# Kernel tuning notes

Hardware: AMD Instinct MI355X
Metric: run time of the kernel (lower is better)

## Reference

```python
import jax, jax.numpy as jnp
import numpy as np

D_MODEL = 1024
NUM_HEADS = 16
D_K = D_MODEL // NUM_HEADS
SCALE = 1.0 / np.sqrt(D_K).astype(np.float32)
MASK_FILL = -10000.0


def setup_inputs() -> dict:
    key = jax.random.key(0)
    ks = jax.random.split(key, 5)
    B, S = 2, 2048
    x = jax.random.normal(ks[0], (B, S, D_MODEL), dtype=jnp.float32)
    mask = jax.random.randint(ks[1], (B, S), 0, 2, dtype=jnp.int32)
    # Kaiming-uniform-ish init like nn.Linear defaults
    lim1 = 1.0 / np.sqrt(D_MODEL)
    Wqkv = jax.random.uniform(ks[2], (D_MODEL, 3 * D_MODEL), jnp.float32, -lim1, lim1)
    bqkv = jnp.zeros((3 * D_MODEL,), jnp.float32)
    Wout = jax.random.uniform(ks[3], (D_MODEL, D_MODEL), jnp.float32, -lim1, lim1)
    bout = jnp.zeros((D_MODEL,), jnp.float32)
    return {"x": x, "mask": mask, "Wqkv": Wqkv, "bqkv": bqkv, "Wout": Wout, "bout": bout}


def reference(x, mask, Wqkv, bqkv, Wout, bout):
    B, S, _ = x.shape
    qkv = (x @ Wqkv + bqkv).reshape(B, S, 3, NUM_HEADS, D_K)
    qkv = jnp.transpose(qkv, (2, 0, 3, 1, 4))
    q, k, v = qkv[0], qkv[1], qkv[2]
    # scaled dot-product scores [B,H,S,S]
    scores = jnp.einsum("bhqd,bhkd->bhqk", q, k) * SCALE
    # key-padding mask [B,S] -> [B,1,1,S]; masked positions set to -10000 (as in source)
    m = mask[:, None, None, :]
    scores = jnp.where(m == 0, MASK_FILL, scores)
    attn = jax.nn.softmax(scores, axis=-1)
    # dropout is disabled (eval/inference)
    context = jnp.einsum("bhqk,bhkd->bhqd", attn, v)
    context = jnp.transpose(context, (0, 2, 1, 3)).reshape(B, S, D_MODEL)
    return context @ Wout + bout
```

## Files before the change

kernel.cpp:

```cpp
#include <hip/hip_runtime.h>

typedef _Float16 f16;
typedef _Float16 f16x2 __attribute__((ext_vector_type(2)));
typedef _Float16 f16x4 __attribute__((ext_vector_type(4)));
typedef _Float16 f16x8 __attribute__((ext_vector_type(8)));
typedef float    f32x4 __attribute__((ext_vector_type(4)));
typedef float    f32x16 __attribute__((ext_vector_type(16)));
typedef int      i32x4 __attribute__((ext_vector_type(4)));

#define NHEADS 16
#define DK 64
#define BATCH 2
#define SEQ 2048
#define DMODEL 1024
#define MTOT (BATCH*SEQ)
#define NQKV (3*DMODEL)
#define NBH  (BATCH*NHEADS)
#define LOG2E 1.44269504f
#define QSCALE (0.125f * LOG2E)
#define MASKVAL (-10000.0f * LOG2E)

__device__ inline f16x8 ld_f16x8_g(const f16* p) {
  return __builtin_bit_cast(f16x8, *reinterpret_cast<const i32x4*>(p));
}

__device__ inline f16x2 cvt_pk(float a, float b) {
  return __builtin_bit_cast(f16x2, __builtin_amdgcn_cvt_pkrtz(a, b));
}

__device__ inline void gl_lds16(const void* g, void* l) {
  __builtin_amdgcn_global_load_lds(
      (const __attribute__((address_space(1))) unsigned int*)g,
      (__attribute__((address_space(3))) unsigned int*)l, 16, 0, 0);
}

__device__ inline int sigma_k(int s) {
  return (s & ~12) | ((s & 4) << 1) | ((s & 8) >> 1);
}

__global__ void k_cvt(const float* __restrict__ in, f16* __restrict__ out, int n) {
  int i = (blockIdx.x * blockDim.x + threadIdx.x) * 4;
  if (i >= n) return;
  float4 v = *reinterpret_cast<const float4*>(in + i);
  f16x4 o = { (f16)v.x, (f16)v.y, (f16)v.z, (f16)v.w };
  *reinterpret_cast<f16x4*>(out + i) = o;
}

__global__ __launch_bounds__(256) void k_scan(const int* __restrict__ mask,
                                              int* __restrict__ cpos,
                                              int* __restrict__ cnt) {
  __shared__ int part[256];
  const int b = blockIdx.x;
  const int t = threadIdx.x;
  const int* mp = mask + b * SEQ;
  int* cp = cpos + b * SEQ;
  const int base = t * 8;
  int m[8]; int s = 0;
  #pragma unroll
  for (int i = 0; i < 8; ++i) { m[i] = mp[base + i]; s += (m[i] != 0); }
  part[t] = s;
  __syncthreads();
  for (int d = 1; d < 256; d <<= 1) {
    int v = (t >= d) ? part[t - d] : 0;
    __syncthreads();
    part[t] += v;
    __syncthreads();
  }
  int pos = (t == 0) ? 0 : part[t - 1];
  #pragma unroll
  for (int i = 0; i < 8; ++i) {
    cp[base + i] = (m[i] != 0) ? pos : -1;
    pos += (m[i] != 0);
  }
  if (t == 255) cnt[b] = part[255];
}

__global__ __launch_bounds__(256) void k_padzero(const int* __restrict__ cnt,
                                                 f16* __restrict__ ko,
                                                 f16* __restrict__ vto) {
  const int bh = blockIdx.x;
  const int b = bh >> 4;
  const int c = cnt[b];
  const int cpad = (c + 63) & ~63;
  const int npad = cpad - c;
  f16* kp = ko + (size_t)bh * SEQ * DK;
  f16* vp = vto + (size_t)bh * DK * SEQ;
  for (int idx = threadIdx.x; idx < npad * DK; idx += 256) {
    int slot = c + idx / DK, d = idx % DK;
    kp[(size_t)slot * DK + d] = (f16)0.f;
    vp[(size_t)d * SEQ + sigma_k(slot)] = (f16)0.f;
  }
}

__global__ void k_tcvt(const float* __restrict__ in, f16* __restrict__ out, int K, int N) {
  __shared__ float tile[32][33];
  int k0 = blockIdx.y * 32, n0 = blockIdx.x * 32;
  int tx = threadIdx.x, ty = threadIdx.y;
  #pragma unroll
  for (int i = 0; i < 4; ++i)
    tile[ty + 8*i][tx] = in[(size_t)(k0 + ty + 8*i) * N + n0 + tx];
  __syncthreads();
  #pragma unroll
  for (int i = 0; i < 4; ++i)
    out[(size_t)(n0 + ty + 8*i) * K + k0 + tx] = (f16)tile[tx][ty + 8*i];
}

__global__ __launch_bounds__(256, 2) void k_gemm_qkv(
    const f16* __restrict__ A, const f16* __restrict__ Bt,
    const float* __restrict__ bias, const int* __restrict__ cpos,
    f16* __restrict__ qo, f16* __restrict__ ko, f16* __restrict__ vto, int K)
{
  __shared__ f16 As[128][64];
  __shared__ f16 Bs[128][64];
  const int m0 = blockIdx.y * 128, n0 = blockIdx.x * 128;
  const int t = threadIdx.x;
  const int l = t & 63, w = t >> 6;
  const int wr = w >> 1, wc = w & 1;
  const int lc = l & 15, g = l >> 4;
  const int srow = l >> 3;
  const int ssl  = ((l & 7) ^ srow) * 16;
  const int swz  = (lc & 7) << 4;

  f32x4 acc[4][4] = {};

  for (int kt = 0; kt < K; kt += 64) {
    __syncthreads();
    #pragma unroll
    for (int it = 0; it < 4; ++it) {
      int row = it*32 + w*8 + srow;
      gl_lds16((const char*)(A  + (size_t)(m0 + row) * K + kt) + ssl,
               &As[it*32 + w*8][0]);
      gl_lds16((const char*)(Bt + (size_t)(n0 + row) * K + kt) + ssl,
               &Bs[it*32 + w*8][0]);
    }
    __syncthreads();

    #pragma unroll
    for (int ks = 0; ks < 64; ks += 32) {
      f16x8 af[4], bf[4];
      #pragma unroll
      for (int i = 0; i < 4; ++i)
        af[i] = *(const f16x8*)((const char*)&As[wr*64 + i*16 + lc][0] + ((ks*2 + g*16) ^ swz));
      #pragma unroll
      for (int j = 0; j < 4; ++j)
        bf[j] = *(const f16x8*)((const char*)&Bs[wc*64 + j*16 + lc][0] + ((ks*2 + g*16) ^ swz));
      #pragma unroll
      for (int i = 0; i < 4; ++i)
        #pragma unroll
        for (int j = 0; j < 4; ++j)
          acc[i][j] = __builtin_amdgcn_mfma_f32_16x16x32_f16(af[i], bf[j], acc[i][j], 0, 0, 0);
    }
  }

  const int which = n0 >> 10;
  #pragma unroll
  for (int i = 0; i < 4; ++i) {
    const int row0 = m0 + wr*64 + i*16 + g*4;
    const int b = row0 >> 11, s0 = row0 & (SEQ - 1);
    int4 cp4 = *reinterpret_cast<const int4*>(cpos + b*SEQ + s0);
    const int cpa[4] = {cp4.x, cp4.y, cp4.z, cp4.w};
    #pragma unroll
    for (int j = 0; j < 4; ++j) {
      const int col = n0 + wc*64 + j*16 + lc;
      const float bv = bias[col];
      const int h = (col >> 6) & 15, d = col & 63;
      const size_t bh = (size_t)(b * NHEADS + h);
      if (which == 0) {
        #pragma unroll
        for (int r = 0; r < 4; ++r)
          qo[(bh * SEQ + s0 + r) * DK + d] = (f16)((acc[i][j][r] + bv) * QSCALE);
      } else if (which == 1) {
        #pragma unroll
        for (int r = 0; r < 4; ++r)
          if (cpa[r] >= 0)
            ko[(bh * SEQ + cpa[r]) * DK + d] = (f16)(acc[i][j][r] + bv);
      } else {
        #pragma unroll
        for (int r = 0; r < 4; ++r)
          if (cpa[r] >= 0)
            vto[(bh * DK + d) * SEQ + sigma_k(cpa[r])] = (f16)(acc[i][j][r] + bv);
      }
    }
  }
}

__global__ __launch_bounds__(256, 2) void k_gemm_out(
    const f16* __restrict__ A, const f16* __restrict__ Bt,
    const float* __restrict__ bias, float* __restrict__ outf, int N, int K)
{
  __shared__ f16 As[64][64];
  __shared__ f16 Bs[128][64];
  const int m0 = blockIdx.y * 64, n0 = blockIdx.x * 128;
  const int t = threadIdx.x;
  const int l = t & 63, w = t >> 6;
  const int lc = l & 15, g = l >> 4;
  const int srow = l >> 3;
  const int ssl  = ((l & 7) ^ srow) * 16;
  const int swz  = (lc & 7) << 4;

  f32x4 acc[4][2] = {};

  for (int kt = 0; kt < K; kt += 64) {
    __syncthreads();
    #pragma unroll
    for (int it = 0; it < 2; ++it) {
      int row = it*32 + w*8 + srow;
      gl_lds16((const char*)(A + (size_t)(m0 + row) * K + kt) + ssl,
               &As[it*32 + w*8][0]);
    }
    #pragma unroll
    for (int it = 0; it < 4; ++it) {
      int row = it*32 + w*8 + srow;
      gl_lds16((const char*)(Bt + (size_t)(n0 + row) * K + kt) + ssl,
               &Bs[it*32 + w*8][0]);
    }
    __syncthreads();

    #pragma unroll
    for (int ks = 0; ks < 64; ks += 32) {
      f16x8 af[4], bf[2];
      #pragma unroll
      for (int i = 0; i < 4; ++i)
        af[i] = *(const f16x8*)((const char*)&As[i*16 + lc][0] + ((ks*2 + g*16) ^ swz));
      #pragma unroll
      for (int j = 0; j < 2; ++j)
        bf[j] = *(const f16x8*)((const char*)&Bs[w*32 + j*16 + lc][0] + ((ks*2 + g*16) ^ swz));
      #pragma unroll
      for (int i = 0; i < 4; ++i)
        #pragma unroll
        for (int j = 0; j < 2; ++j)
          acc[i][j] = __builtin_amdgcn_mfma_f32_16x16x32_f16(af[i], bf[j], acc[i][j], 0, 0, 0);
    }
  }

  #pragma unroll
  for (int i = 0; i < 4; ++i) {
    #pragma unroll
    for (int j = 0; j < 2; ++j) {
      int col = n0 + w*32 + j*16 + lc;
      float bv = bias[col];
      #pragma unroll
      for (int r = 0; r < 4; ++r) {
        int row = m0 + i*16 + g*4 + r;
        outf[(size_t)row * N + col] = acc[i][j][r] + bv;
      }
    }
  }
}

__global__ __launch_bounds__(256, 2) void k_attn10(
    const f16* __restrict__ Q, const f16* __restrict__ K,
    const f16* __restrict__ Vt, const int* __restrict__ cnt,
    f16* __restrict__ ctx)
{
  __shared__ f16 Kb[2][32][128];
  __shared__ f16 Vb[2][32][128];

  const int bid = blockIdx.x;
  const int xcd = bid & 7, slot = bid >> 3;
  const int bh = xcd * 4 + (slot >> 4);
  const int qb = slot & 15;
  const int b  = bh >> 4, h = bh & (NHEADS - 1);
  const int t = threadIdx.x, l = t & 63, w = t >> 6;
  const int r31 = l & 31, hi = l >> 5;
  const int Rm = r31 & 15;
  const int q0 = qb * 128 + w * 32;

  const int c = cnt[b];
  const int NTc = (c + 63) >> 6;

  const f16* Qp = Q + (size_t)bh * SEQ * DK;
  const f16* Kp = K + (size_t)bh * SEQ * DK;
  const f16* Vp = Vt + (size_t)bh * DK * SEQ;

  f16x8 qf[4];
  #pragma unroll
  for (int ds = 0; ds < 4; ++ds)
    qf[ds] = ld_f16x8_g(Qp + (size_t)(q0 + r31) * DK + ds*16 + hi*8);

  f32x16 o[2] = {};
  float mrow = -3e38f;
  float lsum = 0.f;

  auto stage = [&](int buf, int kt) {
    #pragma unroll
    for (int cc = 0; cc < 2; ++cc) {
      int Rbase = w*8 + cc*4;
      int R = Rbase + (l >> 4);
      int u = (l & 15) ^ (R & 15);
      int off32 = (u >> 3) * 32;
      int byteoff = (u & 7) * 16;
      gl_lds16((const char*)Kp + (size_t)(kt + off32 + R) * (DK*2) + byteoff,
               &Kb[buf][Rbase][0]);
      gl_lds16((const char*)Vp + (size_t)(off32 + R) * (SEQ*2) + (size_t)kt*2 + byteoff,
               &Vb[buf][Rbase][0]);
    }
  };

  stage(0, 0);

  for (int it = 0; it < NTc; ++it) {
    __syncthreads();
    if (it + 1 < NTc) stage((it + 1) & 1, (it + 1) * 64);
    const int kt = it * 64;
    const char* kb = (const char*)&Kb[it & 1][0][0];
    const char* vb = (const char*)&Vb[it & 1][0][0];

    f32x16 p[2];
    if (kt + 64 <= c) {
      #pragma unroll
      for (int T = 0; T < 2; ++T)
        #pragma unroll
        for (int r = 0; r < 16; ++r) p[T][r] = 0.f;
    } else {
      #pragma unroll
      for (int T = 0; T < 2; ++T)
        #pragma unroll
        for (int r = 0; r < 16; ++r) {
          int k = kt + T*32 + 4*hi + (r & 3) + 8*(r >> 2);
          p[T][r] = (k < c) ? 0.f : MASKVAL;
        }
    }

    __builtin_amdgcn_s_setprio(1);
    #pragma unroll
    for (int T = 0; T < 2; ++T)
      #pragma unroll
      for (int ds = 0; ds < 4; ++ds) {
        int slotc = T*8 + ds*2 + hi;
        f16x8 kf = *(const f16x8*)(kb + r31*256 + ((slotc ^ Rm) << 4));
        p[T] = __builtin_amdgcn_mfma_f32_32x32x16_f16(kf, qf[ds], p[T], 0, 0, 0);
      }
    __builtin_amdgcn_s_setprio(0);

    float mx;
    {
      f32x4 t4;
      #pragma unroll
      for (int r = 0; r < 4; ++r)
        t4[r] = fmaxf(fmaxf(p[0][r], p[0][r+4]), fmaxf(p[0][r+8], p[0][r+12]));
      #pragma unroll
      for (int r = 0; r < 4; ++r)
        t4[r] = fmaxf(t4[r], fmaxf(fmaxf(p[1][r], p[1][r+4]), fmaxf(p[1][r+8], p[1][r+12])));
      mx = fmaxf(fmaxf(t4[0], t4[1]), fmaxf(t4[2], t4[3]));
    }
    mx = fmaxf(mx, __shfl_xor(mx, 32));

    if (!__all(mx <= mrow + 8.f)) {
      float nm = fmaxf(mrow, mx);
      float sc = __builtin_amdgcn_exp2f(mrow - nm);
      mrow = nm;
      lsum *= sc;
      #pragma unroll
      for (int dt = 0; dt < 2; ++dt)
        #pragma unroll
        for (int r = 0; r < 16; ++r) o[dt][r] *= sc;
    }

    f16x2 h2[2][8];
    float s0 = 0.f, s1 = 0.f;
    #pragma unroll
    for (int T = 0; T < 2; ++T)
      #pragma unroll
      for (int rp = 0; rp < 8; ++rp) {
        float e0 = __builtin_amdgcn_exp2f(p[T][2*rp]   - mrow);
        float e1 = __builtin_amdgcn_exp2f(p[T][2*rp+1] - mrow);
        s0 += e0; s1 += e1;
        h2[T][rp] = cvt_pk(e0, e1);
      }
    lsum += s0 + s1;

    __builtin_amdgcn_s_setprio(1);
    #pragma unroll
    for (int T = 0; T < 2; ++T)
      #pragma unroll
      for (int half = 0; half < 2; ++half) {
        union { f16x2 a[4]; f16x8 v8; } pu;
        pu.a[0] = h2[T][half*4+0]; pu.a[1] = h2[T][half*4+1];
        pu.a[2] = h2[T][half*4+2]; pu.a[3] = h2[T][half*4+3];
        int m = T*2 + half;
        #pragma unroll
        for (int dt = 0; dt < 2; ++dt) {
          int slotc = dt*8 + m*2 + hi;
          f16x8 vf = *(const f16x8*)(vb + r31*256 + ((slotc ^ Rm) << 4));
          o[dt] = __builtin_amdgcn_mfma_f32_32x32x16_f16(vf, pu.v8, o[dt], 0, 0, 0);
        }
      }
    __builtin_amdgcn_s_setprio(0);
  }

  lsum += __shfl_xor(lsum, 32);
  float inv = 1.f / lsum;
  f16* cp = ctx + (size_t)(b*SEQ + q0 + r31) * DMODEL + h*DK;
  #pragma unroll
  for (int dt = 0; dt < 2; ++dt)
    #pragma unroll
    for (int rq = 0; rq < 4; ++rq) {
      union { f16x2 h2v[2]; f16x4 h4v; } u;
      u.h2v[0] = cvt_pk(o[dt][4*rq+0]*inv, o[dt][4*rq+1]*inv);
      u.h2v[1] = cvt_pk(o[dt][4*rq+2]*inv, o[dt][4*rq+3]*inv);
      *(f16x4*)(cp + dt*32 + 8*rq + 4*hi) = u.h4v;
    }
}

extern "C" void kernel_launch(void* const* d_in, const int* in_sizes, int n_in,
                              void* d_out, int out_size, void* d_ws, size_t ws_size,
                              hipStream_t stream) {
  const float* x    = (const float*)d_in[0];
  const int*   mask = (const int*)d_in[1];
  const float* Wqkv = (const float*)d_in[2];
  const float* bqkv = (const float*)d_in[3];
  const float* Wout = (const float*)d_in[4];
  const float* bout = (const float*)d_in[5];
  float* out = (float*)d_out;

  const size_t SZ_X    = (size_t)MTOT * DMODEL * 2;
  const size_t SZ_WQKV = (size_t)NQKV * DMODEL * 2;
  const size_t SZ_WOUT = (size_t)DMODEL * DMODEL * 2;
  const size_t SZ_QKV  = (size_t)BATCH * NHEADS * SEQ * DK * 2;
  const size_t SZ_CP   = (size_t)MTOT * 4;
  const size_t SZ_CNT  = 256;
  const size_t NEED = SZ_X + SZ_WQKV + SZ_WOUT + 3*SZ_QKV + SZ_X + SZ_CP + SZ_CNT;
  if (ws_size < NEED) return;

  char* p = (char*)d_ws;
  f16* xh    = (f16*)p; p += SZ_X;
  f16* Wqkvt = (f16*)p; p += SZ_WQKV;
  f16* Woutt = (f16*)p; p += SZ_WOUT;
  f16* Qh    = (f16*)p; p += SZ_QKV;
  f16* Kh    = (f16*)p; p += SZ_QKV;
  f16* Vth   = (f16*)p; p += SZ_QKV;
  f16* ctx   = (f16*)p; p += SZ_X;
  int* cpos  = (int*)p; p += SZ_CP;
  int* cnt   = (int*)p; p += SZ_CNT;

  k_cvt<<<(MTOT*DMODEL)/(256*4), 256, 0, stream>>>(x, xh, MTOT*DMODEL);
  k_scan<<<BATCH, 256, 0, stream>>>(mask, cpos, cnt);
  k_padzero<<<NBH, 256, 0, stream>>>(cnt, Kh, Vth);
  k_tcvt<<<dim3(NQKV/32, DMODEL/32), dim3(32,8), 0, stream>>>(Wqkv, Wqkvt, DMODEL, NQKV);
  k_tcvt<<<dim3(DMODEL/32, DMODEL/32), dim3(32,8), 0, stream>>>(Wout, Woutt, DMODEL, DMODEL);

  k_gemm_qkv<<<dim3(NQKV/128, MTOT/128), 256, 0, stream>>>(
      xh, Wqkvt, bqkv, cpos, Qh, Kh, Vth, DMODEL);

  k_attn10<<<32 * 16, 256, 0, stream>>>(Qh, Kh, Vth, cnt, ctx);

  k_gemm_out<<<dim3(DMODEL/128, MTOT/64), 256, 0, stream>>>(
      ctx, Woutt, bout, out, DMODEL, DMODEL);
}
```

Before: 110.8 us.

## Compute K/V projection only for unmasked tokens via gather; fuse prep kernels

The QKV GEMM is split into a Q GEMM and a K/V GEMM. The K/V GEMM gathers only the unmasked rows of x through an inverse index built by the scan, and blocks past the padded count exit early. Padding rows are filled with duplicates of the last valid row, which replaces the separate pad-zero kernel. Because those rows now hold real K/V values instead of zeros, correctness depends on the attention kernel ignoring slots beyond the count. The x conversion and both weight transposes are merged into one launch, and V stores are vectorised.

```diff
diff --git a/kernel.cpp b/kernel.cpp
--- a/kernel.cpp
+++ b/kernel.cpp
@@ -38,22 +38,47 @@
   return (s & ~12) | ((s & 4) << 1) | ((s & 8) >> 1);
 }
 
-__global__ void k_cvt(const float* __restrict__ in, f16* __restrict__ out, int n) {
-  int i = (blockIdx.x * blockDim.x + threadIdx.x) * 4;
-  if (i >= n) return;
-  float4 v = *reinterpret_cast<const float4*>(in + i);
-  f16x4 o = { (f16)v.x, (f16)v.y, (f16)v.z, (f16)v.w };
-  *reinterpret_cast<f16x4*>(out + i) = o;
+__device__ inline void tcvt_tile(float (*tile)[33], const float* __restrict__ in,
+                                 f16* __restrict__ out, int K, int N, int k0, int n0) {
+  const int t = threadIdx.x, tx = t & 31, ty = t >> 5;
+  #pragma unroll
+  for (int i = 0; i < 4; ++i)
+    tile[ty + 8*i][tx] = in[(size_t)(k0 + ty + 8*i) * N + n0 + tx];
+  __syncthreads();
+  #pragma unroll
+  for (int i = 0; i < 4; ++i)
+    out[(size_t)(n0 + ty + 8*i) * K + k0 + tx] = (f16)tile[tx][ty + 8*i];
+}
+
+__global__ __launch_bounds__(256) void k_prep(
+    const float* __restrict__ x, f16* __restrict__ xh,
+    const float* __restrict__ Wqkv, f16* __restrict__ Wqkvt,
+    const float* __restrict__ Wout, f16* __restrict__ Woutt)
+{
+  __shared__ float tile[32][33];
+  const int bid = blockIdx.x;
+  if (bid < 4096) {
+    int i = (bid * 256 + threadIdx.x) * 4;
+    float4 v = *reinterpret_cast<const float4*>(x + i);
+    f16x4 o = { (f16)v.x, (f16)v.y, (f16)v.z, (f16)v.w };
+    *reinterpret_cast<f16x4*>(xh + i) = o;
+  } else if (bid < 4096 + 3072) {
+    int tl = bid - 4096;
+    tcvt_tile(tile, Wqkv, Wqkvt, DMODEL, NQKV, (tl / 96) * 32, (tl % 96) * 32);
+  } else {
+    int tl = bid - 4096 - 3072;
+    tcvt_tile(tile, Wout, Woutt, DMODEL, DMODEL, (tl / 32) * 32, (tl % 32) * 32);
+  }
 }
 
 __global__ __launch_bounds__(256) void k_scan(const int* __restrict__ mask,
-                                              int* __restrict__ cpos,
+                                              int* __restrict__ inv,
                                               int* __restrict__ cnt) {
   __shared__ int part[256];
   const int b = blockIdx.x;
   const int t = threadIdx.x;
   const int* mp = mask + b * SEQ;
-  int* cp = cpos + b * SEQ;
+  int* iv = inv + b * SEQ;
   const int base = t * 8;
   int m[8]; int s = 0;
   #pragma unroll
@@ -69,67 +94,38 @@
   int pos = (t == 0) ? 0 : part[t - 1];
   #pragma unroll
   for (int i = 0; i < 8; ++i) {
-    cp[base + i] = (m[i] != 0) ? pos : -1;
-    pos += (m[i] != 0);
+    if (m[i] != 0) { iv[pos] = base + i; ++pos; }
   }
   if (t == 255) cnt[b] = part[255];
 }
 
-__global__ __launch_bounds__(256) void k_padzero(const int* __restrict__ cnt,
-                                                 f16* __restrict__ ko,
-                                                 f16* __restrict__ vto) {
-  const int bh = blockIdx.x;
-  const int b = bh >> 4;
-  const int c = cnt[b];
-  const int cpad = (c + 63) & ~63;
-  const int npad = cpad - c;
-  f16* kp = ko + (size_t)bh * SEQ * DK;
-  f16* vp = vto + (size_t)bh * DK * SEQ;
-  for (int idx = threadIdx.x; idx < npad * DK; idx += 256) {
-    int slot = c + idx / DK, d = idx % DK;
-    kp[(size_t)slot * DK + d] = (f16)0.f;
-    vp[(size_t)d * SEQ + sigma_k(slot)] = (f16)0.f;
-  }
-}
-
-__global__ void k_tcvt(const float* __restrict__ in, f16* __restrict__ out, int K, int N) {
-  __shared__ float tile[32][33];
-  int k0 = blockIdx.y * 32, n0 = blockIdx.x * 32;
-  int tx = threadIdx.x, ty = threadIdx.y;
-  #pragma unroll
-  for (int i = 0; i < 4; ++i)
-    tile[ty + 8*i][tx] = in[(size_t)(k0 + ty + 8*i) * N + n0 + tx];
-  __syncthreads();
-  #pragma unroll
-  for (int i = 0; i < 4; ++i)
-    out[(size_t)(n0 + ty + 8*i) * K + k0 + tx] = (f16)tile[tx][ty + 8*i];
-}
-
-__global__ __launch_bounds__(256, 2) void k_gemm_qkv(
+__global__ __launch_bounds__(256, 2) void k_gemm_q(
     const f16* __restrict__ A, const f16* __restrict__ Bt,
-    const float* __restrict__ bias, const int* __restrict__ cpos,
-    f16* __restrict__ qo, f16* __restrict__ ko, f16* __restrict__ vto, int K)
+    const float* __restrict__ bias, f16* __restrict__ qo, int K)
 {
-  __shared__ f16 As[128][64];
+  __shared__ f16 As[64][64];
   __shared__ f16 Bs[128][64];
-  const int m0 = blockIdx.y * 128, n0 = blockIdx.x * 128;
+  const int m0 = blockIdx.y * 64, n0 = blockIdx.x * 128;
   const int t = threadIdx.x;
   const int l = t & 63, w = t >> 6;
-  const int wr = w >> 1, wc = w & 1;
   const int lc = l & 15, g = l >> 4;
   const int srow = l >> 3;
   const int ssl  = ((l & 7) ^ srow) * 16;
   const int swz  = (lc & 7) << 4;
 
-  f32x4 acc[4][4] = {};
+  f32x4 acc[4][2] = {};
 
   for (int kt = 0; kt < K; kt += 64) {
     __syncthreads();
+    #pragma unroll
+    for (int it = 0; it < 2; ++it) {
+      int row = it*32 + w*8 + srow;
+      gl_lds16((const char*)(A + (size_t)(m0 + row) * K + kt) + ssl,
+               &As[it*32 + w*8][0]);
+    }
     #pragma unroll
     for (int it = 0; it < 4; ++it) {
       int row = it*32 + w*8 + srow;
-      gl_lds16((const char*)(A  + (size_t)(m0 + row) * K + kt) + ssl,
-               &As[it*32 + w*8][0]);
       gl_lds16((const char*)(Bt + (size_t)(n0 + row) * K + kt) + ssl,
                &Bs[it*32 + w*8][0]);
     }
@@ -137,48 +133,119 @@
 
     #pragma unroll
     for (int ks = 0; ks < 64; ks += 32) {
-      f16x8 af[4], bf[4];
+      f16x8 af[4], bf[2];
       #pragma unroll
       for (int i = 0; i < 4; ++i)
-        af[i] = *(const f16x8*)((const char*)&As[wr*64 + i*16 + lc][0] + ((ks*2 + g*16) ^ swz));
-      #pragma unroll
-      for (int j = 0; j < 4; ++j)
-        bf[j] = *(const f16x8*)((const char*)&Bs[wc*64 + j*16 + lc][0] + ((ks*2 + g*16) ^ swz));
+        af[i] = *(const f16x8*)((const char*)&As[i*16 + lc][0] + ((ks*2 + g*16) ^ swz));
+      #pragma unroll
+      for (int j = 0; j < 2; ++j)
+        bf[j] = *(const f16x8*)((const char*)&Bs[w*32 + j*16 + lc][0] + ((ks*2 + g*16) ^ swz));
       #pragma unroll
       for (int i = 0; i < 4; ++i)
         #pragma unroll
-        for (int j = 0; j < 4; ++j)
+        for (int j = 0; j < 2; ++j)
           acc[i][j] = __builtin_amdgcn_mfma_f32_16x16x32_f16(af[i], bf[j], acc[i][j], 0, 0, 0);
     }
   }
 
-  const int which = n0 >> 10;
   #pragma unroll
   for (int i = 0; i < 4; ++i) {
-    const int row0 = m0 + wr*64 + i*16 + g*4;
+    const int row0 = m0 + i*16 + g*4;
     const int b = row0 >> 11, s0 = row0 & (SEQ - 1);
-    int4 cp4 = *reinterpret_cast<const int4*>(cpos + b*SEQ + s0);
-    const int cpa[4] = {cp4.x, cp4.y, cp4.z, cp4.w};
-    #pragma unroll
-    for (int j = 0; j < 4; ++j) {
-      const int col = n0 + wc*64 + j*16 + lc;
-      const float bv = bias[col];
-      const int h = (col >> 6) & 15, d = col & 63;
-      const size_t bh = (size_t)(b * NHEADS + h);
-      if (which == 0) {
+    #pragma unroll
+    for (int j = 0; j < 2; ++j) {
+      int col = n0 + w*32 + j*16 + lc;
+      float bv = bias[col];
+      int h = col >> 6, d = col & 63;
+      size_t bh = (size_t)(b * NHEADS + h);
+      #pragma unroll
+      for (int r = 0; r < 4; ++r)
+        qo[(bh * SEQ + s0 + r) * DK + d] = (f16)((acc[i][j][r] + bv) * QSCALE);
+    }
+  }
+}
+
+__global__ __launch_bounds__(256, 2) void k_gemm_kv(
+    const f16* __restrict__ A, const f16* __restrict__ Bt,
+    const float* __restrict__ bias, const int* __restrict__ inv,
+    const int* __restrict__ cnt,
+    f16* __restrict__ ko, f16* __restrict__ vto, int K)
+{
+  __shared__ f16 As[64][64];
+  __shared__ f16 Bs[128][64];
+  const int m0 = blockIdx.y * 64;
+  const int n0 = blockIdx.x * 128;
+  const int b = m0 >> 11, sl0 = m0 & (SEQ - 1);
+  const int c = cnt[b];
+  if (sl0 >= ((c + 63) & ~63)) return;
+
+  const int t = threadIdx.x;
+  const int l = t & 63, w = t >> 6;
+  const int lc = l & 15, g = l >> 4;
+  const int srow = l >> 3;
+  const int ssl  = ((l & 7) ^ srow) * 16;
+  const int swz  = (lc & 7) << 4;
+
+  int orig[2];
+  #pragma unroll
+  for (int it = 0; it < 2; ++it) {
+    int slot = sl0 + it*32 + w*8 + srow;
+    int sidx = (slot < c) ? slot : (c > 0 ? c - 1 : 0);
+    orig[it] = inv[b * SEQ + sidx] & (SEQ - 1);
+  }
+
+  f32x4 acc[4][2] = {};
+
+  for (int kt = 0; kt < K; kt += 64) {
+    __syncthreads();
+    #pragma unroll
+    for (int it = 0; it < 2; ++it)
+      gl_lds16((const char*)(A + ((size_t)(b * SEQ + orig[it])) * K + kt) + ssl,
+               &As[it*32 + w*8][0]);
+    #pragma unroll
+    for (int it = 0; it < 4; ++it) {
+      int row = it*32 + w*8 + srow;
+      gl_lds16((const char*)(Bt + (size_t)(n0 + row) * K + kt) + ssl,
+               &Bs[it*32 + w*8][0]);
+    }
+    __syncthreads();
+
+    #pragma unroll
+    for (int ks = 0; ks < 64; ks += 32) {
+      f16x8 af[4], bf[2];
+      #pragma unroll
+      for (int i = 0; i < 4; ++i)
+        af[i] = *(const f16x8*)((const char*)&As[i*16 + lc][0] + ((ks*2 + g*16) ^ swz));
+      #pragma unroll
+      for (int j = 0; j < 2; ++j)
+        bf[j] = *(const f16x8*)((const char*)&Bs[w*32 + j*16 + lc][0] + ((ks*2 + g*16) ^ swz));
+      #pragma unroll
+      for (int i = 0; i < 4; ++i)
+        #pragma unroll
+        for (int j = 0; j < 2; ++j)
+          acc[i][j] = __builtin_amdgcn_mfma_f32_16x16x32_f16(af[i], bf[j], acc[i][j], 0, 0, 0);
+    }
+  }
+
+  #pragma unroll
+  for (int i = 0; i < 4; ++i) {
+    const int slot0 = sl0 + i*16 + g*4;
+    #pragma unroll
+    for (int j = 0; j < 2; ++j) {
+      int colkv = n0 + w*32 + j*16 + lc;
+      float bv = bias[colkv];
+      int kv = colkv >> 10;
+      int h = (colkv >> 6) & 15, d = colkv & 63;
+      size_t bh = (size_t)(b * NHEADS + h);
+      if (kv == 0) {
         #pragma unroll
         for (int r = 0; r < 4; ++r)
-          qo[(bh * SEQ + s0 + r) * DK + d] = (f16)((acc[i][j][r] + bv) * QSCALE);
-      } else if (which == 1) {
-        #pragma unroll
-        for (int r = 0; r < 4; ++r)
-          if (cpa[r] >= 0)
-            ko[(bh * SEQ + cpa[r]) * DK + d] = (f16)(acc[i][j][r] + bv);
+          ko[(bh * SEQ + slot0 + r) * DK + d] = (f16)(acc[i][j][r] + bv);
       } else {
-        #pragma unroll
-        for (int r = 0; r < 4; ++r)
-          if (cpa[r] >= 0)
-            vto[(bh * DK + d) * SEQ + sigma_k(cpa[r])] = (f16)(acc[i][j][r] + bv);
+        union { f16x2 h2[2]; f16x4 h4; } u;
+        u.h2[0] = cvt_pk(acc[i][j][0] + bv, acc[i][j][1] + bv);
+        u.h2[1] = cvt_pk(acc[i][j][2] + bv, acc[i][j][3] + bv);
+        *(f16x4*)(vto + (bh * DK + d) * SEQ + sigma_k(slot0)) = u.h4;
       }
     }
   }
@@ -418,9 +485,9 @@
   const size_t SZ_WQKV = (size_t)NQKV * DMODEL * 2;
   const size_t SZ_WOUT = (size_t)DMODEL * DMODEL * 2;
   const size_t SZ_QKV  = (size_t)BATCH * NHEADS * SEQ * DK * 2;
-  const size_t SZ_CP   = (size_t)MTOT * 4;
+  const size_t SZ_INV  = (size_t)MTOT * 4;
   const size_t SZ_CNT  = 256;
-  const size_t NEED = SZ_X + SZ_WQKV + SZ_WOUT + 3*SZ_QKV + SZ_X + SZ_CP + SZ_CNT;
+  const size_t NEED = SZ_X + SZ_WQKV + SZ_WOUT + 3*SZ_QKV + SZ_X + SZ_INV + SZ_CNT;
   if (ws_size < NEED) return;
 
   char* p = (char*)d_ws;
@@ -431,17 +498,16 @@
   f16* Kh    = (f16*)p; p += SZ_QKV;
   f16* Vth   = (f16*)p; p += SZ_QKV;
   f16* ctx   = (f16*)p; p += SZ_X;
-  int* cpos  = (int*)p; p += SZ_CP;
+  int* inv   = (int*)p; p += SZ_INV;
   int* cnt   = (int*)p; p += SZ_CNT;
 
-  k_cvt<<<(MTOT*DMODEL)/(256*4), 256, 0, stream>>>(x, xh, MTOT*DMODEL);
-  k_scan<<<BATCH, 256, 0, stream>>>(mask, cpos, cnt);
-  k_padzero<<<NBH, 256, 0, stream>>>(cnt, Kh, Vth);
-  k_tcvt<<<dim3(NQKV/32, DMODEL/32), dim3(32,8), 0, stream>>>(Wqkv, Wqkvt, DMODEL, NQKV);
-  k_tcvt<<<dim3(DMODEL/32, DMODEL/32), dim3(32,8), 0, stream>>>(Wout, Woutt, DMODEL, DMODEL);
-
-  k_gemm_qkv<<<dim3(NQKV/128, MTOT/128), 256, 0, stream>>>(
-      xh, Wqkvt, bqkv, cpos, Qh, Kh, Vth, DMODEL);
+  k_prep<<<4096 + 3072 + 1024, 256, 0, stream>>>(x, xh, Wqkv, Wqkvt, Wout, Woutt);
+  k_scan<<<BATCH, 256, 0, stream>>>(mask, inv, cnt);
+
+  k_gemm_q<<<dim3(DMODEL/128, MTOT/64), 256, 0, stream>>>(
+      xh, Wqkvt, bqkv, Qh, DMODEL);
+  k_gemm_kv<<<dim3(2048/128, MTOT/64), 256, 0, stream>>>(
+      xh, Wqkvt + (size_t)DMODEL*DMODEL, bqkv + DMODEL, inv, cnt, Kh, Vth, DMODEL);
 
   k_attn10<<<32 * 16, 256, 0, stream>>>(Qh, Kh, Vth, cnt, ctx);
 
```

Measured after the change: 104.0 us. -6.1%, faster.
